# Optimization experiments

Hardware: AMD Instinct MI355X
Metric: run time of the kernel (lower is better)

## Reference

```python
import jax, jax.numpy as jnp
import numpy as np

DIM = 512
HEADS = 8
D_HEAD = 64
INNER = HEADS * D_HEAD  # 512
CTX_DIM = 768
FF_INNER = 4 * DIM  # 2048
SCALE = D_HEAD ** -0.5
LN_EPS = 1e-5


def layer_norm(x, g, b):
    mu = jnp.mean(x, axis=-1, keepdims=True)
    var = jnp.var(x, axis=-1, keepdims=True)
    return (x - mu) * jax.lax.rsqrt(var + LN_EPS) * g + b


def attention(x, ctx, qw, kw, vw, ow, ob):
    B, N, _ = x.shape
    M = ctx.shape[1]
    q = (x @ qw).reshape(B, N, HEADS, D_HEAD).transpose(0, 2, 1, 3)
    k = (ctx @ kw).reshape(B, M, HEADS, D_HEAD).transpose(0, 2, 1, 3)
    v = (ctx @ vw).reshape(B, M, HEADS, D_HEAD).transpose(0, 2, 1, 3)
    sim = jnp.einsum('bhid,bhjd->bhij', q, k) * SCALE  # [B,H,N,M]
    attn = jax.nn.softmax(sim, axis=-1)
    out = jnp.einsum('bhij,bhjd->bhid', attn, v)
    out = out.transpose(0, 2, 1, 3).reshape(B, N, INNER)
    return out @ ow + ob


def setup_inputs() -> dict:
    key = jax.random.key(0)
    ks = jax.random.split(key, 20)
    r = lambda k, shp, s=0.02: jax.random.normal(k, shp, dtype=jnp.float32) * s
    return {
        'x': jax.random.normal(ks[0], (2, 4096, DIM), dtype=jnp.float32),
        'context': jax.random.normal(ks[1], (2, 256, CTX_DIM), dtype=jnp.float32),
        'q1_w': r(ks[2], (DIM, INNER)), 'k1_w': r(ks[3], (DIM, INNER)),
        'v1_w': r(ks[4], (DIM, INNER)), 'o1_w': r(ks[5], (INNER, DIM)),
        'o1_b': jnp.zeros((DIM,), jnp.float32),
        'q2_w': r(ks[6], (DIM, INNER)), 'k2_w': r(ks[7], (CTX_DIM, INNER)),
        'v2_w': r(ks[8], (CTX_DIM, INNER)), 'o2_w': r(ks[9], (INNER, DIM)),
        'o2_b': jnp.zeros((DIM,), jnp.float32),
        'ff_in_w': r(ks[10], (DIM, 2 * FF_INNER)), 'ff_in_b': jnp.zeros((2 * FF_INNER,), jnp.float32),
        'ff_out_w': r(ks[11], (FF_INNER, DIM)), 'ff_out_b': jnp.zeros((DIM,), jnp.float32),
        'ln1_g': jnp.ones((DIM,), jnp.float32), 'ln1_b': jnp.zeros((DIM,), jnp.float32),
        'ln2_g': jnp.ones((DIM,), jnp.float32), 'ln2_b': jnp.zeros((DIM,), jnp.float32),
        'ln3_g': jnp.ones((DIM,), jnp.float32), 'ln3_b': jnp.zeros((DIM,), jnp.float32),
    }


def reference(x, context, q1_w, k1_w, v1_w, o1_w, o1_b,
              q2_w, k2_w, v2_w, o2_w, o2_b,
              ff_in_w, ff_in_b, ff_out_w, ff_out_b,
              ln1_g, ln1_b, ln2_g, ln2_b, ln3_g, ln3_b):
    # self-attention + residual
    h = layer_norm(x, ln1_g, ln1_b)
    x = attention(h, h, q1_w, k1_w, v1_w, o1_w, o1_b) + x
    # cross-attention + residual
    h = layer_norm(x, ln2_g, ln2_b)
    x = attention(h, context, q2_w, k2_w, v2_w, o2_w, o2_b) + x
    # GEGLU feed-forward + residual (torch F.gelu is exact erf form)
    h = layer_norm(x, ln3_g, ln3_b)
    proj = h @ ff_in_w + ff_in_b
    val, gate = jnp.split(proj, 2, axis=-1)
    ff = (val * jax.nn.gelu(gate, approximate=False)) @ ff_out_w + ff_out_b
    return ff + x
```

## Files before the change

kernel.cpp:

```cpp
#include <hip/hip_runtime.h>
#include <hip/hip_bf16.h>
#include <cstdint>


typedef __bf16 bf16_t;
typedef __bf16 bf16x8 __attribute__((ext_vector_type(8)));
typedef float f32x4 __attribute__((ext_vector_type(4)));
typedef float f32x16 __attribute__((ext_vector_type(16)));
typedef unsigned int u32x4 __attribute__((ext_vector_type(4)));

__device__ __forceinline__ bf16_t f2bf(float f) { return (bf16_t)f; }

__device__ __forceinline__ f32x4 mfma16(bf16x8 a, bf16x8 b, f32x4 c) {
  return __builtin_amdgcn_mfma_f32_16x16x32_bf16(a, b, c, 0, 0, 0);
}
__device__ __forceinline__ f32x16 mfma32(bf16x8 a, bf16x8 b, f32x16 c) {
  return __builtin_amdgcn_mfma_f32_32x32x16_bf16(a, b, c, 0, 0, 0);
}

__device__ __forceinline__ float gelu_exact(float x) {
  return 0.5f * x * (1.0f + erff(x * 0.70710678118654752f));
}

__device__ __forceinline__ void gload_lds16(const bf16_t* g, bf16_t* lds) {
  __builtin_amdgcn_global_load_lds(
      (const __attribute__((address_space(1))) unsigned int*)g,
      (__attribute__((address_space(3))) unsigned int*)lds, 16, 0, 0);
}

__global__ __launch_bounds__(256) void ln_kernel(const float* __restrict__ in,
                                                 const float* __restrict__ gw,
                                                 const float* __restrict__ bw,
                                                 bf16_t* __restrict__ out) {
  int w = threadIdx.x >> 6, l = threadIdx.x & 63;
  size_t row = (size_t)blockIdx.x * 4 + w;
  const float* p = in + row * 512 + l * 8;
  f32x4 va = *(const f32x4*)p;
  f32x4 vb = *(const f32x4*)(p + 4);
  float xs[8] = {va[0], va[1], va[2], va[3], vb[0], vb[1], vb[2], vb[3]};
  float s = 0.f;
#pragma unroll
  for (int j = 0; j < 8; j++) s += xs[j];
#pragma unroll
  for (int m = 1; m < 64; m <<= 1) s += __shfl_xor(s, m);
  float mu = s * (1.0f / 512.0f);
  float v = 0.f;
#pragma unroll
  for (int j = 0; j < 8; j++) { float d = xs[j] - mu; v += d * d; }
#pragma unroll
  for (int m = 1; m < 64; m <<= 1) v += __shfl_xor(v, m);
  float rstd = rsqrtf(v * (1.0f / 512.0f) + 1e-5f);
  f32x4 g0 = *(const f32x4*)(gw + l * 8);
  f32x4 g1 = *(const f32x4*)(gw + l * 8 + 4);
  f32x4 b0 = *(const f32x4*)(bw + l * 8);
  f32x4 b1 = *(const f32x4*)(bw + l * 8 + 4);
  bf16x8 o;
#pragma unroll
  for (int j = 0; j < 4; j++) o[j] = f2bf((xs[j] - mu) * rstd * g0[j] + b0[j]);
#pragma unroll
  for (int j = 0; j < 4; j++) o[4 + j] = f2bf((xs[4 + j] - mu) * rstd * g1[j] + b1[j]);
  *(bf16x8*)(out + row * 512 + l * 8) = o;
}

__global__ __launch_bounds__(256) void wtrans_kernel(const float* __restrict__ W,
                                                     bf16_t* __restrict__ Wt,
                                                     int K, int N, float sc) {
  __shared__ float t[32][33];
  int k0 = blockIdx.x * 32, n0 = blockIdx.y * 32;
#pragma unroll
  for (int i = 0; i < 4; i++) {
    int idx = threadIdx.x + i * 256;
    int kk = idx >> 5, nn = idx & 31;
    t[kk][nn] = W[(size_t)(k0 + kk) * N + n0 + nn];
  }
  __syncthreads();
#pragma unroll
  for (int i = 0; i < 4; i++) {
    int idx = threadIdx.x + i * 256;
    int nn = idx >> 5, kk = idx & 31;
    Wt[(size_t)(n0 + nn) * K + k0 + kk] = f2bf(t[kk][nn] * sc);
  }
}

__global__ __launch_bounds__(256) void cvt_kernel(const float* __restrict__ in,
                                                  bf16_t* __restrict__ out) {
  int i = (blockIdx.x * 256 + threadIdx.x) * 4;
  f32x4 v = *(const f32x4*)(in + i);
  out[i + 0] = f2bf(v[0]);
  out[i + 1] = f2bf(v[1]);
  out[i + 2] = f2bf(v[2]);
  out[i + 3] = f2bf(v[3]);
}

template <int BM, int BN, int EPI>
__global__ __launch_bounds__(256) void gemm_kernel(
    const bf16_t* __restrict__ A, const bf16_t* __restrict__ Bt,
    const float* __restrict__ bias, const float* __restrict__ res,
    void* __restrict__ outp, int M, int N, int K, int gateOff, int ldo) {
  constexpr int WR = BM / 2;
  constexpr int WN = BN / 2;
  constexpr int MF = WR / 16;
  constexpr int NF = WN / 16;
  constexpr int ABLK = BM / 64;
  constexpr int BROWS = (EPI == 2) ? 2 * BN : BN;
  constexpr int BBLK = BROWS / 64;
  __shared__ bf16_t Al[2][BM][32];
  __shared__ bf16_t Bl[2][BROWS][32];

  int tid = threadIdx.x;
  int w = tid >> 6, l = tid & 63;
  int wr = w >> 1, wc = w & 1;
  int lg = l >> 4, lc = l & 15;
  int m0 = blockIdx.x * BM, n0 = blockIdx.y * BN;

  f32x4 acc[MF][NF] = {};
  f32x4 acc2[MF][NF] = {};

  int srow = tid >> 2, scol = (tid & 3) * 8;
  const bf16_t* aP[ABLK];
#pragma unroll
  for (int i = 0; i < ABLK; i++)
    aP[i] = A + (size_t)(m0 + i * 64 + srow) * K + scol;
  const bf16_t* bP[BBLK];
  if (EPI == 2) {
    bP[0] = Bt + (size_t)(n0 + srow) * K + scol;
    bP[1] = Bt + (size_t)(n0 + gateOff + srow) * K + scol;
  } else {
#pragma unroll
    for (int i = 0; i < BBLK; i++)
      bP[i] = Bt + (size_t)(n0 + i * 64 + srow) * K + scol;
  }

  auto STAGE = [&](int buf, int k0) {
#pragma unroll
    for (int i = 0; i < ABLK; i++)
      gload_lds16(aP[i] + k0, &Al[buf][i * 64 + w * 16][0]);
#pragma unroll
    for (int i = 0; i < BBLK; i++)
      gload_lds16(bP[i] + k0, &Bl[buf][i * 64 + w * 16][0]);
  };

  int nk = K / 32;
  int cur = 0;
  STAGE(0, 0);
  __syncthreads();

  for (int t = 0; t < nk; ++t) {
    if (t + 1 < nk) STAGE(cur ^ 1, (t + 1) * 32);

    bf16x8 af[MF];
#pragma unroll
    for (int mi = 0; mi < MF; mi++)
      af[mi] = *(const bf16x8*)&Al[cur][wr * WR + mi * 16 + lc][lg * 8];
    bf16x8 bfr[NF];
#pragma unroll
    for (int ni = 0; ni < NF; ni++)
      bfr[ni] = *(const bf16x8*)&Bl[cur][wc * WN + ni * 16 + lc][lg * 8];
#pragma unroll
    for (int mi = 0; mi < MF; mi++)
#pragma unroll
      for (int ni = 0; ni < NF; ni++)
        acc[mi][ni] = mfma16(af[mi], bfr[ni], acc[mi][ni]);
    if (EPI == 2) {
      bf16x8 bg[NF];
#pragma unroll
      for (int ni = 0; ni < NF; ni++)
        bg[ni] = *(const bf16x8*)&Bl[cur][BN + wc * WN + ni * 16 + lc][lg * 8];
#pragma unroll
      for (int mi = 0; mi < MF; mi++)
#pragma unroll
        for (int ni = 0; ni < NF; ni++)
          acc2[mi][ni] = mfma16(af[mi], bg[ni], acc2[mi][ni]);
    }
    __syncthreads();
    cur ^= 1;
  }

#pragma unroll
  for (int mi = 0; mi < MF; mi++) {
#pragma unroll
    for (int ni = 0; ni < NF; ni++) {
#pragma unroll
      for (int r = 0; r < 4; r++) {
        int row = m0 + wr * WR + mi * 16 + lg * 4 + r;
        int col = n0 + wc * WN + ni * 16 + lc;
        float v = acc[mi][ni][r];
        if (EPI == 0) {
          ((bf16_t*)outp)[(size_t)row * ldo + col] = f2bf(v);
        } else if (EPI == 3) {
          int cs = (col & ~15) | (lc & 3) | ((lc & 4) << 1) | ((lc & 8) >> 1);
          ((bf16_t*)outp)[(size_t)row * ldo + cs] = f2bf(v);
        } else if (EPI == 1) {
          ((float*)outp)[(size_t)row * ldo + col] =
              v + bias[col] + res[(size_t)row * ldo + col];
        } else {
          float g = acc2[mi][ni][r] + bias[col + gateOff];
          float val = v + bias[col];
          ((bf16_t*)outp)[(size_t)row * ldo + col] = f2bf(val * gelu_exact(g));
        }
      }
    }
  }
}

__global__ __launch_bounds__(256) void attn_kernel(
    const bf16_t* __restrict__ Q, int ldq, const bf16_t* __restrict__ Kb,
    int ldk, const bf16_t* __restrict__ Vt, bf16_t* __restrict__ O, int Mkv) {
  __shared__ bf16_t Klds[64][72];
  __shared__ bf16_t Vlds[64][72];

  int qt = blockIdx.x, head = blockIdx.y, b = blockIdx.z;
  int tid = threadIdx.x;
  int w = tid >> 6, l = tid & 63;
  int ql = l & 31, hi = l >> 5;
  int ldv = 2 * Mkv;

  size_t qrow = (size_t)b * 4096 + qt * 128 + w * 32 + ql;
  const bf16_t* qp = Q + qrow * ldq + head * 64 + hi * 8;
  bf16x8 qf[4];
#pragma unroll
  for (int dk = 0; dk < 4; dk++) qf[dk] = *(const bf16x8*)(qp + dk * 16);

  f32x16 o0 = {}, o1 = {};
  f32x16 zacc = {};
  float mrun = -1e30f;

  bf16x8 vones;
#pragma unroll
  for (int j = 0; j < 8; j++) vones[j] = f2bf(1.0f);

  int key0 = tid >> 2, dc0 = (tid & 3) * 16;
  const bf16_t* kp = Kb + ((size_t)b * Mkv + key0) * ldk + head * 64 + dc0;
  const bf16_t* vp = Vt + (size_t)(head * 64 + key0) * ldv + b * Mkv + dc0;

  bf16x8 kc0 = *(const bf16x8*)kp, kc1 = *(const bf16x8*)(kp + 8);
  bf16x8 vc0 = *(const bf16x8*)vp, vc1 = *(const bf16x8*)(vp + 8);

  for (int t0 = 0; t0 < Mkv; t0 += 64) {
    __syncthreads();
    *(bf16x8*)&Klds[key0][dc0] = kc0;
    *(bf16x8*)&Klds[key0][dc0 + 8] = kc1;
    *(bf16x8*)&Vlds[key0][dc0] = vc0;
    *(bf16x8*)&Vlds[key0][dc0 + 8] = vc1;
    __syncthreads();

    if (t0 + 64 < Mkv) {
      kp += (size_t)64 * ldk;
      vp += 64;
      kc0 = *(const bf16x8*)kp;
      kc1 = *(const bf16x8*)(kp + 8);
      vc0 = *(const bf16x8*)vp;
      vc1 = *(const bf16x8*)(vp + 8);
    }

    f32x16 s0 = {}, s1 = {};
    __builtin_amdgcn_s_setprio(1);
#pragma unroll
    for (int dk = 0; dk < 4; dk++) {
      bf16x8 a0 = *(const bf16x8*)&Klds[ql][dk * 16 + hi * 8];
      bf16x8 a1 = *(const bf16x8*)&Klds[32 + ql][dk * 16 + hi * 8];
      s0 = mfma32(a0, qf[dk], s0);
      s1 = mfma32(a1, qf[dk], s1);
    }
    __builtin_amdgcn_s_setprio(0);

    float tmax = s0[0];
#pragma unroll
    for (int r = 1; r < 16; r++) tmax = fmaxf(tmax, s0[r]);
#pragma unroll
    for (int r = 0; r < 16; r++) tmax = fmaxf(tmax, s1[r]);
    tmax = fmaxf(tmax, __shfl_xor(tmax, 32));

    if (!__all(tmax <= mrun + 8.0f)) {
      float mnew = fmaxf(mrun, tmax);
      float resc = __builtin_amdgcn_exp2f(mrun - mnew);
      mrun = mnew;
#pragma unroll
      for (int r = 0; r < 16; r++) {
        float f = __shfl(resc, (r & 3) + 8 * (r >> 2) + 4 * hi);
        o0[r] *= f;
        o1[r] *= f;
        zacc[r] *= f;
      }
    }

    bf16x8 pa[4];
#pragma unroll
    for (int m = 0; m < 4; m++) {
#pragma unroll
      for (int j = 0; j < 8; j++) {
        float sv = (m < 2) ? s0[(m & 1) * 8 + j] : s1[(m & 1) * 8 + j];
        pa[m][j] = f2bf(__builtin_amdgcn_exp2f(sv - mrun));
      }
    }

    __builtin_amdgcn_s_setprio(1);
#pragma unroll
    for (int m = 0; m < 4; m++) {
      zacc = mfma32(pa[m], vones, zacc);
      bf16x8 vb0 = *(const bf16x8*)&Vlds[ql][m * 16 + hi * 8];
      bf16x8 vb1 = *(const bf16x8*)&Vlds[32 + ql][m * 16 + hi * 8];
      o0 = mfma32(pa[m], vb0, o0);
      o1 = mfma32(pa[m], vb1, o1);
    }
    __builtin_amdgcn_s_setprio(0);
  }

  size_t ob = ((size_t)b * 4096 + qt * 128 + w * 32) * 512 + head * 64;
#pragma unroll
  for (int r = 0; r < 16; r++) {
    float inv = 1.0f / zacc[r];
    int q = (r & 3) + 8 * (r >> 2) + 4 * hi;
    O[ob + (size_t)q * 512 + ql] = f2bf(o0[r] * inv);
    O[ob + (size_t)q * 512 + 32 + ql] = f2bf(o1[r] * inv);
  }
}

extern "C" void kernel_launch(void* const* d_in, const int* in_sizes, int n_in,
                              void* d_out, int out_size, void* d_ws,
                              size_t ws_size, hipStream_t stream) {
  const float* x = (const float*)d_in[0];
  const float* ctx = (const float*)d_in[1];
  const float* q1_w = (const float*)d_in[2];
  const float* k1_w = (const float*)d_in[3];
  const float* v1_w = (const float*)d_in[4];
  const float* o1_w = (const float*)d_in[5];
  const float* o1_b = (const float*)d_in[6];
  const float* q2_w = (const float*)d_in[7];
  const float* k2_w = (const float*)d_in[8];
  const float* v2_w = (const float*)d_in[9];
  const float* o2_w = (const float*)d_in[10];
  const float* o2_b = (const float*)d_in[11];
  const float* ff_in_w = (const float*)d_in[12];
  const float* ff_in_b = (const float*)d_in[13];
  const float* ff_out_w = (const float*)d_in[14];
  const float* ff_out_b = (const float*)d_in[15];
  const float* ln1_g = (const float*)d_in[16];
  const float* ln1_b = (const float*)d_in[17];
  const float* ln2_g = (const float*)d_in[18];
  const float* ln2_b = (const float*)d_in[19];
  const float* ln3_g = (const float*)d_in[20];
  const float* ln3_b = (const float*)d_in[21];

  char* ws = (char*)d_ws;
  float* xr = (float*)(ws + 0);
  bf16_t* hb = (bf16_t*)(ws + 16777216);
  bf16_t* qkb = (bf16_t*)(ws + 25165824);
  bf16_t* ao = (bf16_t*)(ws + 41943040);
  bf16_t* ffmid = qkb;
  bf16_t* kb = (bf16_t*)(ws + 50331648);
  bf16_t* vtg2 = (bf16_t*)(ws + 50855936);
  bf16_t* ctxb = (bf16_t*)(ws + 51380224);
  bf16_t* wts = (bf16_t*)(ws + 58720256);
  bf16_t* vtg = (bf16_t*)(ws + 69730304);

  bf16_t* q1t = wts + 0;
  bf16_t* k1t = wts + 262144;
  bf16_t* v1t = wts + 524288;
  bf16_t* o1t = wts + 786432;
  bf16_t* q2t = wts + 1048576;
  bf16_t* k2t = wts + 1310720;
  bf16_t* v2t = wts + 1703936;
  bf16_t* o2t = wts + 2097152;
  bf16_t* ffint = wts + 2359296;
  bf16_t* ffoutt = wts + 4456448;

  const float QS = 0.125f * 1.44269504f;

  wtrans_kernel<<<dim3(16, 16), 256, 0, stream>>>(q1_w, q1t, 512, 512, QS);
  wtrans_kernel<<<dim3(16, 16), 256, 0, stream>>>(k1_w, k1t, 512, 512, 1.0f);
  wtrans_kernel<<<dim3(16, 16), 256, 0, stream>>>(v1_w, v1t, 512, 512, 1.0f);
  wtrans_kernel<<<dim3(16, 16), 256, 0, stream>>>(o1_w, o1t, 512, 512, 1.0f);
  wtrans_kernel<<<dim3(16, 16), 256, 0, stream>>>(q2_w, q2t, 512, 512, QS);
  wtrans_kernel<<<dim3(24, 16), 256, 0, stream>>>(k2_w, k2t, 768, 512, 1.0f);
  wtrans_kernel<<<dim3(24, 16), 256, 0, stream>>>(v2_w, v2t, 768, 512, 1.0f);
  wtrans_kernel<<<dim3(16, 16), 256, 0, stream>>>(o2_w, o2t, 512, 512, 1.0f);
  wtrans_kernel<<<dim3(16, 128), 256, 0, stream>>>(ff_in_w, ffint, 512, 4096, 1.0f);
  wtrans_kernel<<<dim3(64, 16), 256, 0, stream>>>(ff_out_w, ffoutt, 2048, 512, 1.0f);
  cvt_kernel<<<384, 256, 0, stream>>>(ctx, ctxb);

  ln_kernel<<<2048, 256, 0, stream>>>(x, ln1_g, ln1_b, hb);
  gemm_kernel<128, 128, 0><<<dim3(64, 8), 256, 0, stream>>>(
      hb, q1t, nullptr, nullptr, qkb, 8192, 1024, 512, 0, 1024);
  gemm_kernel<64, 128, 3><<<dim3(8, 64), 256, 0, stream>>>(
      v1t, hb, nullptr, nullptr, vtg, 512, 8192, 512, 0, 8192);
  attn_kernel<<<dim3(32, 8, 2), 256, 0, stream>>>(qkb, 1024, qkb + 512, 1024,
                                                  vtg, ao, 4096);
  gemm_kernel<64, 128, 1><<<dim3(128, 4), 256, 0, stream>>>(
      ao, o1t, o1_b, x, xr, 8192, 512, 512, 0, 512);

  ln_kernel<<<2048, 256, 0, stream>>>(xr, ln2_g, ln2_b, hb);
  gemm_kernel<64, 128, 0><<<dim3(128, 4), 256, 0, stream>>>(
      hb, q2t, nullptr, nullptr, qkb, 8192, 512, 512, 0, 512);
  gemm_kernel<64, 128, 0><<<dim3(8, 4), 256, 0, stream>>>(
      ctxb, k2t, nullptr, nullptr, kb, 512, 512, 768, 0, 512);
  gemm_kernel<64, 128, 3><<<dim3(8, 4), 256, 0, stream>>>(
      v2t, ctxb, nullptr, nullptr, vtg2, 512, 512, 768, 0, 512);
  attn_kernel<<<dim3(32, 8, 2), 256, 0, stream>>>(qkb, 512, kb, 512, vtg2, ao,
                                                  256);
  gemm_kernel<64, 128, 1><<<dim3(128, 4), 256, 0, stream>>>(
      ao, o2t, o2_b, xr, xr, 8192, 512, 512, 0, 512);

  ln_kernel<<<2048, 256, 0, stream>>>(xr, ln3_g, ln3_b, hb);
  gemm_kernel<128, 64, 2><<<dim3(64, 32), 256, 0, stream>>>(
      hb, ffint, ff_in_b, nullptr, ffmid, 8192, 2048, 512, 2048, 2048);
  gemm_kernel<64, 128, 1><<<dim3(128, 4), 256, 0, stream>>>(
      ffmid, ffoutt, ff_out_b, xr, (float*)d_out, 8192, 512, 2048, 0, 512);
}
```

Baseline: 335.6 us.

## Batch weight transposes into one launch and deepen GEMM K-step to 64

Ten separate weight transpose/convert launches are merged into one kernel that looks up its job from a table by block index, cutting launch overhead and tail gaps. Separately, the GEMM main loop now stages 64 K-elements per iteration as two 32-wide halves, halving the number of barriers and loop iterations. The price is double the shared memory per block, which may lower occupancy, especially for the GEGLU variant with doubled B rows. All GEMM K values (512, 768, 2048) divide by 64.

```diff
diff --git a/kernel.cpp b/kernel.cpp
--- a/kernel.cpp
+++ b/kernel.cpp
@@ -7,7 +7,6 @@
 typedef __bf16 bf16x8 __attribute__((ext_vector_type(8)));
 typedef float f32x4 __attribute__((ext_vector_type(4)));
 typedef float f32x16 __attribute__((ext_vector_type(16)));
-typedef unsigned int u32x4 __attribute__((ext_vector_type(4)));
 
 __device__ __forceinline__ bf16_t f2bf(float f) { return (bf16_t)f; }
 
@@ -62,23 +61,41 @@
   *(bf16x8*)(out + row * 512 + l * 8) = o;
 }
 
-__global__ __launch_bounds__(256) void wtrans_kernel(const float* __restrict__ W,
-                                                     bf16_t* __restrict__ Wt,
-                                                     int K, int N, float sc) {
+struct WJob {
+  const float* W;
+  bf16_t* Wt;
+  int K;
+  int N;
+  float sc;
+  int tile0;
+};
+struct WJobs {
+  WJob j[10];
+};
+
+__global__ __launch_bounds__(256) void wtrans_all_kernel(WJobs jobs) {
   __shared__ float t[32][33];
-  int k0 = blockIdx.x * 32, n0 = blockIdx.y * 32;
-#pragma unroll
-  for (int i = 0; i < 4; i++) {
-    int idx = threadIdx.x + i * 256;
+  int bid = blockIdx.x;
+  int i = 0;
+#pragma unroll
+  for (int q = 1; q < 10; q++)
+    if (bid >= jobs.j[q].tile0) i = q;
+  WJob jb = jobs.j[i];
+  int tt = bid - jb.tile0;
+  int ktiles = jb.K >> 5;
+  int k0 = (tt % ktiles) * 32, n0 = (tt / ktiles) * 32;
+#pragma unroll
+  for (int s = 0; s < 4; s++) {
+    int idx = threadIdx.x + s * 256;
     int kk = idx >> 5, nn = idx & 31;
-    t[kk][nn] = W[(size_t)(k0 + kk) * N + n0 + nn];
+    t[kk][nn] = jb.W[(size_t)(k0 + kk) * jb.N + n0 + nn];
   }
   __syncthreads();
 #pragma unroll
-  for (int i = 0; i < 4; i++) {
-    int idx = threadIdx.x + i * 256;
+  for (int s = 0; s < 4; s++) {
+    int idx = threadIdx.x + s * 256;
     int nn = idx >> 5, kk = idx & 31;
-    Wt[(size_t)(n0 + nn) * K + k0 + kk] = f2bf(t[kk][nn] * sc);
+    jb.Wt[(size_t)(n0 + nn) * jb.K + k0 + kk] = f2bf(t[kk][nn] * jb.sc);
   }
 }
 
@@ -104,8 +121,8 @@
   constexpr int ABLK = BM / 64;
   constexpr int BROWS = (EPI == 2) ? 2 * BN : BN;
   constexpr int BBLK = BROWS / 64;
-  __shared__ bf16_t Al[2][BM][32];
-  __shared__ bf16_t Bl[2][BROWS][32];
+  __shared__ bf16_t Al[2][2][BM][32];
+  __shared__ bf16_t Bl[2][2][BROWS][32];
 
   int tid = threadIdx.x;
   int w = tid >> 6, l = tid & 63;
@@ -133,44 +150,51 @@
 
   auto STAGE = [&](int buf, int k0) {
 #pragma unroll
-    for (int i = 0; i < ABLK; i++)
-      gload_lds16(aP[i] + k0, &Al[buf][i * 64 + w * 16][0]);
-#pragma unroll
-    for (int i = 0; i < BBLK; i++)
-      gload_lds16(bP[i] + k0, &Bl[buf][i * 64 + w * 16][0]);
+    for (int kh = 0; kh < 2; kh++) {
+#pragma unroll
+      for (int i = 0; i < ABLK; i++)
+        gload_lds16(aP[i] + k0 + kh * 32, &Al[buf][kh][i * 64 + w * 16][0]);
+#pragma unroll
+      for (int i = 0; i < BBLK; i++)
+        gload_lds16(bP[i] + k0 + kh * 32, &Bl[buf][kh][i * 64 + w * 16][0]);
+    }
   };
 
-  int nk = K / 32;
+  int nk = K / 64;
   int cur = 0;
   STAGE(0, 0);
   __syncthreads();
 
   for (int t = 0; t < nk; ++t) {
-    if (t + 1 < nk) STAGE(cur ^ 1, (t + 1) * 32);
-
-    bf16x8 af[MF];
-#pragma unroll
-    for (int mi = 0; mi < MF; mi++)
-      af[mi] = *(const bf16x8*)&Al[cur][wr * WR + mi * 16 + lc][lg * 8];
-    bf16x8 bfr[NF];
-#pragma unroll
-    for (int ni = 0; ni < NF; ni++)
-      bfr[ni] = *(const bf16x8*)&Bl[cur][wc * WN + ni * 16 + lc][lg * 8];
-#pragma unroll
-    for (int mi = 0; mi < MF; mi++)
+    if (t + 1 < nk) STAGE(cur ^ 1, (t + 1) * 64);
+
+#pragma unroll
+    for (int kh = 0; kh < 2; kh++) {
+      bf16x8 af[MF];
+#pragma unroll
+      for (int mi = 0; mi < MF; mi++)
+        af[mi] = *(const bf16x8*)&Al[cur][kh][wr * WR + mi * 16 + lc][lg * 8];
+      bf16x8 bfr[NF];
 #pragma unroll
       for (int ni = 0; ni < NF; ni++)
-        acc[mi][ni] = mfma16(af[mi], bfr[ni], acc[mi][ni]);
-    if (EPI == 2) {
-      bf16x8 bg[NF];
-#pragma unroll
-      for (int ni = 0; ni < NF; ni++)
-        bg[ni] = *(const bf16x8*)&Bl[cur][BN + wc * WN + ni * 16 + lc][lg * 8];
+        bfr[ni] = *(const bf16x8*)&Bl[cur][kh][wc * WN + ni * 16 + lc][lg * 8];
 #pragma unroll
       for (int mi = 0; mi < MF; mi++)
 #pragma unroll
         for (int ni = 0; ni < NF; ni++)
-          acc2[mi][ni] = mfma16(af[mi], bg[ni], acc2[mi][ni]);
+          acc[mi][ni] = mfma16(af[mi], bfr[ni], acc[mi][ni]);
+      if (EPI == 2) {
+        bf16x8 bg[NF];
+#pragma unroll
+        for (int ni = 0; ni < NF; ni++)
+          bg[ni] =
+              *(const bf16x8*)&Bl[cur][kh][BN + wc * WN + ni * 16 + lc][lg * 8];
+#pragma unroll
+        for (int mi = 0; mi < MF; mi++)
+#pragma unroll
+          for (int ni = 0; ni < NF; ni++)
+            acc2[mi][ni] = mfma16(af[mi], bg[ni], acc2[mi][ni]);
+      }
     }
     __syncthreads();
     cur ^= 1;
@@ -367,16 +391,22 @@
 
   const float QS = 0.125f * 1.44269504f;
 
-  wtrans_kernel<<<dim3(16, 16), 256, 0, stream>>>(q1_w, q1t, 512, 512, QS);
-  wtrans_kernel<<<dim3(16, 16), 256, 0, stream>>>(k1_w, k1t, 512, 512, 1.0f);
-  wtrans_kernel<<<dim3(16, 16), 256, 0, stream>>>(v1_w, v1t, 512, 512, 1.0f);
-  wtrans_kernel<<<dim3(16, 16), 256, 0, stream>>>(o1_w, o1t, 512, 512, 1.0f);
-  wtrans_kernel<<<dim3(16, 16), 256, 0, stream>>>(q2_w, q2t, 512, 512, QS);
-  wtrans_kernel<<<dim3(24, 16), 256, 0, stream>>>(k2_w, k2t, 768, 512, 1.0f);
-  wtrans_kernel<<<dim3(24, 16), 256, 0, stream>>>(v2_w, v2t, 768, 512, 1.0f);
-  wtrans_kernel<<<dim3(16, 16), 256, 0, stream>>>(o2_w, o2t, 512, 512, 1.0f);
-  wtrans_kernel<<<dim3(16, 128), 256, 0, stream>>>(ff_in_w, ffint, 512, 4096, 1.0f);
-  wtrans_kernel<<<dim3(64, 16), 256, 0, stream>>>(ff_out_w, ffoutt, 2048, 512, 1.0f);
+  WJobs jobs;
+  auto setj = [&](int i, const float* W, bf16_t* Wt, int K, int N, float sc,
+                  int tile0) {
+    jobs.j[i] = WJob{W, Wt, K, N, sc, tile0};
+  };
+  setj(0, q1_w, q1t, 512, 512, QS, 0);
+  setj(1, k1_w, k1t, 512, 512, 1.0f, 256);
+  setj(2, v1_w, v1t, 512, 512, 1.0f, 512);
+  setj(3, o1_w, o1t, 512, 512, 1.0f, 768);
+  setj(4, q2_w, q2t, 512, 512, QS, 1024);
+  setj(5, k2_w, k2t, 768, 512, 1.0f, 1280);
+  setj(6, v2_w, v2t, 768, 512, 1.0f, 1664);
+  setj(7, o2_w, o2t, 512, 512, 1.0f, 2048);
+  setj(8, ff_in_w, ffint, 512, 4096, 1.0f, 2304);
+  setj(9, ff_out_w, ffoutt, 2048, 512, 1.0f, 4352);
+  wtrans_all_kernel<<<5376, 256, 0, stream>>>(jobs);
   cvt_kernel<<<384, 256, 0, stream>>>(ctx, ctxb);
 
   ln_kernel<<<2048, 256, 0, stream>>>(x, ln1_g, ln1_b, hb);
```

Result: faster. 307.8 us (-8.3%).
